# Optimization experiments

Hardware: AMD Instinct MI355X
Metric: run time of the kernel (lower is better)

## Reference

```python
import jax, jax.numpy as jnp
import numpy as np

BN_EPS = 1e-5


def three_nn(unknown, known):
    # squared pairwise distances via gemm form: ||u||^2 + ||k||^2 - 2 u.k
    # unknown: (B, n, 3), known: (B, m, 3) -> d: (B, n, m)
    u2 = jnp.sum(unknown * unknown, axis=-1, keepdims=True)          # (B, n, 1)
    k2 = jnp.sum(known * known, axis=-1)[:, None, :]                 # (B, 1, m)
    d = u2 + k2 - 2.0 * jnp.einsum('bnc,bmc->bnm', unknown, known)   # (B, n, m)
    neg_d, idx = jax.lax.top_k(-d, 3)                                # 3 smallest
    return -neg_d, idx                                               # (B,n,3), (B,n,3) int32


def three_interpolate(known_feats, idx, weight):
    # known_feats: (B, C, m), idx/weight: (B, n, 3) -> (B, C, n)
    g = jnp.take_along_axis(known_feats[:, :, None, :], idx[:, None, :, :], axis=3)  # (B,C,n,3)
    return jnp.sum(g * weight[:, None, :, :], axis=3)


def conv1x1(x, W, b):
    # x: (B, C_in, N), W: (C_out, C_in), b: (C_out,)
    return jnp.einsum('oc,bcn->bon', W, x) + b[None, :, None]


def batchnorm(x, gamma, beta):
    # training-mode BN over (B, N) per channel, biased variance
    mean = jnp.mean(x, axis=(0, 2), keepdims=True)
    var = jnp.mean((x - mean) ** 2, axis=(0, 2), keepdims=True)
    xn = (x - mean) * jax.lax.rsqrt(var + BN_EPS)
    return xn * gamma[None, :, None] + beta[None, :, None]


def setup_inputs() -> dict:
    key = jax.random.key(0)
    ks = jax.random.split(key, 16)
    B, n, m = 16, 4096, 1024
    C1, C2, C = 128, 256, 256  # in_channels, known feat channels (=mlp[0]), mlp width
    inp = {
        'unknown': jax.random.normal(ks[0], (B, n, 3), jnp.float32),
        'known': jax.random.normal(ks[1], (B, m, 3), jnp.float32),
        'unknow_feats': jax.random.normal(ks[2], (B, C1, n), jnp.float32),
        'known_feats': jax.random.normal(ks[3], (B, C2, m), jnp.float32),
        # mlp_unknow: Conv1d(C1->C) + BN (no relu)
        'Wu': jax.random.normal(ks[4], (C, C1), jnp.float32) * (1.0 / np.sqrt(C1)),
        'bu': jnp.zeros((C,), jnp.float32),
        'gu': jnp.ones((C,), jnp.float32),
        'betau': jnp.zeros((C,), jnp.float32),
        # mlp_convs[0]: Conv1d(C->C) + BN + relu
        'W1': jax.random.normal(ks[5], (C, C), jnp.float32) * (1.0 / np.sqrt(C)),
        'b1': jnp.zeros((C,), jnp.float32),
        'g1': jnp.ones((C,), jnp.float32),
        'beta1': jnp.zeros((C,), jnp.float32),
        # mlp_convs[1]: Conv1d(C->C) + BN + relu
        'W2': jax.random.normal(ks[6], (C, C), jnp.float32) * (1.0 / np.sqrt(C)),
        'b2': jnp.zeros((C,), jnp.float32),
        'g2': jnp.ones((C,), jnp.float32),
        'beta2': jnp.zeros((C,), jnp.float32),
    }
    return inp


def reference(unknown, known, unknow_feats, known_feats,
              Wu, bu, gu, betau, W1, b1, g1, beta1, W2, b2, g2, beta2):
    dist, idx = three_nn(unknown, known)            # squared dists (B,n,3)
    dist_recip = 1.0 / (dist + 1e-8)
    norm = jnp.sum(dist_recip, axis=2, keepdims=True)
    weight = dist_recip / norm
    interpolated = three_interpolate(known_feats, idx, weight)   # (B, 256, n)

    skip = batchnorm(conv1x1(unknow_feats, Wu, bu), gu, betau)   # (B, 256, n)
    x = interpolated + skip
    x = jax.nn.relu(batchnorm(conv1x1(x, W1, b1), g1, beta1))
    x = jax.nn.relu(batchnorm(conv1x1(x, W2, b2), g2, beta2))
    return x
```

## Files before the change

### kernel.cpp

```cpp
#include <hip/hip_runtime.h>
#include <hip/hip_bf16.h>
#include <cstddef>
#include <cstdint>

#define BATCH 16
#define NPTS  4096
#define MPTS  1024
#define PTOT  65536
#define C1    128
#define C2    256

typedef short bf16x8 __attribute__((ext_vector_type(8)));
typedef float f32x4  __attribute__((ext_vector_type(4)));
typedef unsigned int u32x4 __attribute__((ext_vector_type(4)));

static __device__ __forceinline__ float bf2f(unsigned int u16) {
    union { unsigned int i; float f; } v; v.i = u16 << 16; return v.f;
}
static __device__ __forceinline__ unsigned short f2bf(float f) {
    union { float f; unsigned int i; } v; v.f = f;
    unsigned int u = v.i;
    return (unsigned short)((u + 0x7FFFu + ((u >> 16) & 1u)) >> 16);
}

static __device__ __forceinline__ void st_wt_b128(void* p, u32x4 v) {
    asm volatile("global_store_dwordx4 %0, %1, off sc0 sc1" :: "v"(p), "v"(v) : "memory");
}
static __device__ __forceinline__ void st_wt_f128(void* p, f32x4 v) {
    asm volatile("global_store_dwordx4 %0, %1, off sc0 sc1" :: "v"(p), "v"(v) : "memory");
}
static __device__ __forceinline__ void st_wt_b32(void* p, unsigned v) {
    asm volatile("global_store_dword %0, %1, off sc0 sc1" :: "v"(p), "v"(v) : "memory");
}
static __device__ __forceinline__ void st_wt_b16(void* p, unsigned v) {
    asm volatile("global_store_short %0, %1, off sc0 sc1" :: "v"(p), "v"(v) : "memory");
}

template <int SWZ>
__global__ void k_transpose(const float* __restrict__ in, unsigned short* __restrict__ out,
                            int C, int N) {
    __shared__ float tile[64][65];
    int b  = blockIdx.z;
    int n0 = blockIdx.x * 64;
    int c0 = blockIdx.y * 64;
    const float* src = in + (size_t)b * C * N;
    unsigned short* dst = out + (size_t)b * N * C;
    int t  = threadIdx.x;
    int t4 = t >> 6;
    int tn = t & 63;
#pragma unroll
    for (int i = 0; i < 16; ++i) {
        int cc = i * 4 + t4;
        tile[cc][tn] = src[(size_t)(c0 + cc) * N + n0 + tn];
    }
    __syncthreads();
#pragma unroll
    for (int i = 0; i < 16; ++i) {
        int nn = i * 4 + t4;
        int p  = n0 + nn;
        int c  = c0 + tn;
        size_t off;
        if (SWZ) off = (size_t)p * C + (size_t)((((c >> 3) ^ (p & 7)) << 3) + (c & 7));
        else     off = (size_t)p * C + c;
        st_wt_b16(dst + off, (unsigned)f2bf(tile[tn][nn]));
    }
}

__global__ void k_cvt_pack(const float* __restrict__ in, unsigned short* __restrict__ out, int K) {
    int tid = blockIdx.x * 256 + threadIdx.x;
    if (tid >= 256 * K) return;
    int ch = tid / K, k = tid % K;
    int ks = k >> 5, lhi = (k >> 3) & 3, e = k & 7;
    int wv = ch >> 6, i = (ch >> 4) & 3, llo = ch & 15;
    int lane = lhi * 16 + llo;
    st_wt_b16(out + ((size_t)((ks * 16 + wv * 4 + i) * 64 + lane)) * 8 + e,
              (unsigned)f2bf(in[tid]));
}

static __device__ __forceinline__ bool nn_less(float da, int ia, float db, int ib) {
    return (da < db) || (da == db && ia < ib);
}

__global__ void k_three_nn(const float* __restrict__ unknown, const float* __restrict__ known,
                           int* __restrict__ idx_out, float* __restrict__ w_out) {
    __shared__ float4 kpt[MPTS + 8];
    int t  = threadIdx.x;
    int p0 = blockIdx.x * 32;
    int b  = p0 >> 12;
    const float* kb = known + (size_t)b * MPTS * 3;
    for (int i = t; i < MPTS; i += 256) {
        float x = kb[i * 3 + 0], y = kb[i * 3 + 1], z = kb[i * 3 + 2];
        float dd = __fadd_rn(__fadd_rn(__fmul_rn(x, x), __fmul_rn(y, y)), __fmul_rn(z, z));
        float4 v; v.x = x; v.y = y; v.z = z; v.w = dd;
        kpt[i + (i >> 7)] = v;
    }
    __syncthreads();

    int q = t & 7;
    int p = p0 + (t >> 3);
    const float* up = unknown + (size_t)p * 3;
    float ux = up[0], uy = up[1], uz = up[2];
    float u2 = __fadd_rn(__fadd_rn(__fmul_rn(ux, ux), __fmul_rn(uy, uy)), __fmul_rn(uz, uz));

    float d0 = INFINITY, d1 = INFINITY, d2 = INFINITY;
    int   i0 = 0, i1 = 0, i2 = 0;
    int base = q * 129;
#pragma unroll 4
    for (int it = 0; it < 128; ++it) {
        float4 kp = kpt[base + it];
        float dot = __fadd_rn(__fadd_rn(__fmul_rn(ux, kp.x), __fmul_rn(uy, kp.y)),
                              __fmul_rn(uz, kp.z));
        float d = __fsub_rn(__fadd_rn(u2, kp.w), __fmul_rn(2.0f, dot));
        int k = q * 128 + it;
        if (d < d0)      { d2 = d1; i2 = i1; d1 = d0; i1 = i0; d0 = d; i0 = k; }
        else if (d < d1) { d2 = d1; i2 = i1; d1 = d;  i1 = k; }
        else if (d < d2) { d2 = d;  i2 = k; }
    }

#pragma unroll
    for (int m = 1; m <= 4; m <<= 1) {
        float e0 = __shfl_xor(d0, m, 64), e1 = __shfl_xor(d1, m, 64), e2 = __shfl_xor(d2, m, 64);
        int   j0 = __shfl_xor(i0, m, 64), j1 = __shfl_xor(i1, m, 64), j2 = __shfl_xor(i2, m, 64);
        float a0 = d0, a1 = d1, a2 = d2; int x0 = i0, x1 = i1, x2 = i2;
        float b0 = e0, b1 = e1, b2 = e2; int y0 = j0, y1 = j1, y2 = j2;
        bool tk = nn_less(a0, x0, b0, y0);
        d0 = tk ? a0 : b0; i0 = tk ? x0 : y0;
        float na0 = tk ? a1 : a0; int nx0 = tk ? x1 : x0;
        float na1 = tk ? a2 : a1; int nx1 = tk ? x2 : x1;
        float nb0 = tk ? b0 : b1; int ny0 = tk ? y0 : y1;
        float nb1 = tk ? b1 : b2; int ny1 = tk ? y1 : y2;
        tk = nn_less(na0, nx0, nb0, ny0);
        d1 = tk ? na0 : nb0; i1 = tk ? nx0 : ny0;
        float ma0 = tk ? na1 : na0; int mx0 = tk ? nx1 : nx0;
        float mb0 = tk ? nb0 : nb1; int my0 = tk ? ny0 : ny1;
        tk = nn_less(ma0, mx0, mb0, my0);
        d2 = tk ? ma0 : mb0; i2 = tk ? mx0 : my0;
    }

    if (q == 0) {
        float r0 = 1.0f / (d0 + 1e-8f), r1 = 1.0f / (d1 + 1e-8f), r2 = 1.0f / (d2 + 1e-8f);
        float norm = r0 + r1 + r2;
        size_t pg = (size_t)p;
        st_wt_b32(idx_out + pg * 3 + 0, (unsigned)i0);
        st_wt_b32(idx_out + pg * 3 + 1, (unsigned)i1);
        st_wt_b32(idx_out + pg * 3 + 2, (unsigned)i2);
        union { float f; unsigned u; } w0v, w1v, w2v;
        w0v.f = r0 / norm; w1v.f = r1 / norm; w2v.f = r2 / norm;
        st_wt_b32(w_out + pg * 3 + 0, w0v.u);
        st_wt_b32(w_out + pg * 3 + 1, w1v.u);
        st_wt_b32(w_out + pg * 3 + 2, w2v.u);
    }
}

template <int K, int MODE>
__global__ __launch_bounds__(256, 4) void k_gemm(
        const unsigned short* __restrict__ Wp,
        const unsigned short* __restrict__ X,
        const float* __restrict__ Xf,
        const unsigned short* __restrict__ kfT,
        const int* __restrict__ idx,
        const float* __restrict__ wgt,
        const float* __restrict__ bias,
        const float* __restrict__ aff_a,
        const float* __restrict__ aff_c,
        unsigned short* __restrict__ Y,
        float* __restrict__ partial) {
    constexpr int NK = K / 32;
    constexpr int TB = 16 * K * 2;
    __shared__ char smem[8192];

    const int t    = threadIdx.x;
    const int p0   = blockIdx.x * 16;
    const int wv   = t >> 6;
    const int lane = t & 63;
    const int lhi  = lane >> 4, llo = lane & 15;

    if (MODE == 0) {
        const char* src = (const char*)(X + (size_t)p0 * K);
        constexpr int ITERS = TB / (256 * 16);
#pragma unroll
        for (int i = 0; i < ITERS; ++i) {
            int off = (i * 256 + t) * 16;
            __builtin_amdgcn_global_load_lds(
                (const __attribute__((address_space(1))) unsigned int*)(src + off),
                (__attribute__((address_space(3))) unsigned int*)(smem + off),
                16, 0, 0);
        }
    } else if (MODE == 1) {
        constexpr int CPR = K / 8;
#pragma unroll
        for (int i = 0; i < (16 * CPR) / 256; ++i) {
            int f   = i * 256 + t;
            int row = f / CPR, qp = f % CPR;
            int col = qp ^ (row & 7);
            uint4 v = *(const uint4*)(X + (size_t)(p0 + row) * K + qp * 8);
            unsigned int w[4] = {v.x, v.y, v.z, v.w};
            float4 a0 = *(const float4*)(aff_a + col * 8);
            float4 a1 = *(const float4*)(aff_a + col * 8 + 4);
            float4 cc0 = *(const float4*)(aff_c + col * 8);
            float4 cc1 = *(const float4*)(aff_c + col * 8 + 4);
            float aa[8] = {a0.x, a0.y, a0.z, a0.w, a1.x, a1.y, a1.z, a1.w};
            float cc[8] = {cc0.x, cc0.y, cc0.z, cc0.w, cc1.x, cc1.y, cc1.z, cc1.w};
#pragma unroll
            for (int q2 = 0; q2 < 4; ++q2) {
                float lo = fmaxf(bf2f(w[q2] & 0xffff) * aa[q2 * 2]     + cc[q2 * 2],     0.0f);
                float hi = fmaxf(bf2f(w[q2] >> 16)    * aa[q2 * 2 + 1] + cc[q2 * 2 + 1], 0.0f);
                w[q2] = (unsigned int)f2bf(lo) | ((unsigned int)f2bf(hi) << 16);
            }
            uint4 o; o.x = w[0]; o.y = w[1]; o.z = w[2]; o.w = w[3];
            *(uint4*)(smem + row * (K * 2) + qp * 16) = o;
        }
    } else if (MODE == 2) {
        int c    = t >> 1;
        int half = (t & 1) * 8;
        int b    = p0 >> 12;
        const float* src = Xf + ((size_t)b * C1 + c) * NPTS + (p0 & 4095) + half;
        float4 v0 = *(const float4*)(src);
        float4 v1 = *(const float4*)(src + 4);
        float fv[8] = {v0.x, v0.y, v0.z, v0.w, v1.x, v1.y, v1.z, v1.w};
#pragma unroll
        for (int e = 0; e < 8; ++e) {
            int p = half + e;
            *(unsigned short*)(smem + p * (K * 2) +
                               ((((c >> 3) ^ (p & 7)) << 4) + (c & 7) * 2)) = f2bf(fv[e]);
        }
    } else {
        int pj  = t >> 4;
        int sub = t & 15;
        int p   = p0 + pj;
        int b   = p >> 12;
        int i0 = idx[p * 3 + 0], i1 = idx[p * 3 + 1], i2 = idx[p * 3 + 2];
        float w0 = wgt[p * 3 + 0], w1 = wgt[p * 3 + 1], w2 = wgt[p * 3 + 2];
        const unsigned short* kb = kfT + (size_t)b * MPTS * C2;
#pragma unroll
        for (int cc2 = 0; cc2 < 2; ++cc2) {
            int cc = sub * 2 + cc2;
            int cbase = cc * 8;
            u32x4 v0 = *(const u32x4*)(kb + (size_t)i0 * C2 + cbase);
            u32x4 v1 = *(const u32x4*)(kb + (size_t)i1 * C2 + cbase);
            u32x4 v2 = *(const u32x4*)(kb + (size_t)i2 * C2 + cbase);
            int pos = cc ^ (p & 7);
            u32x4 vy = *(const u32x4*)(X + (size_t)p * C2 + pos * 8);
            float4 a0 = *(const float4*)(aff_a + cbase);
            float4 a1 = *(const float4*)(aff_a + cbase + 4);
            float4 c0f = *(const float4*)(aff_c + cbase);
            float4 c1f = *(const float4*)(aff_c + cbase + 4);
            float aa[8] = {a0.x, a0.y, a0.z, a0.w, a1.x, a1.y, a1.z, a1.w};
            float cf[8] = {c0f.x, c0f.y, c0f.z, c0f.w, c1f.x, c1f.y, c1f.z, c1f.w};
            unsigned r[4];
#pragma unroll
            for (int qq = 0; qq < 4; ++qq) {
                float lo = w0 * bf2f(v0[qq] & 0xffff) + w1 * bf2f(v1[qq] & 0xffff)
                         + w2 * bf2f(v2[qq] & 0xffff)
                         + bf2f(vy[qq] & 0xffff) * aa[qq * 2] + cf[qq * 2];
                float hi = w0 * bf2f(v0[qq] >> 16) + w1 * bf2f(v1[qq] >> 16)
                         + w2 * bf2f(v2[qq] >> 16)
                         + bf2f(vy[qq] >> 16) * aa[qq * 2 + 1] + cf[qq * 2 + 1];
                r[qq] = (unsigned)f2bf(lo) | ((unsigned)f2bf(hi) << 16);
            }
            u32x4 vo; vo.x = r[0]; vo.y = r[1]; vo.z = r[2]; vo.w = r[3];
            *(u32x4*)(smem + pj * 512 + pos * 16) = vo;
        }
    }

    const unsigned short* wbase = Wp + ((size_t)(wv * 256) + lane) * 8;
    bf16x8 wA[4], wB[4];
#pragma unroll
    for (int i = 0; i < 4; ++i)
        wA[i] = *(const bf16x8*)(wbase + i * 512);

    __syncthreads();

    f32x4 acc[4];
#pragma unroll
    for (int i = 0; i < 4; ++i) acc[i] = (f32x4){0.f, 0.f, 0.f, 0.f};

#pragma unroll
    for (int ks = 0; ks < NK; ks += 2) {
#pragma unroll
        for (int i = 0; i < 4; ++i)
            wB[i] = *(const bf16x8*)(wbase + (size_t)(ks + 1) * 8192 + i * 512);
        {
            int cp = (ks * 4 + lhi) ^ (llo & 7);
            bf16x8 bb = *(const bf16x8*)(smem + llo * (K * 2) + cp * 16);
#pragma unroll
            for (int i = 0; i < 4; ++i)
                acc[i] = __builtin_amdgcn_mfma_f32_16x16x32_bf16(wA[i], bb, acc[i], 0, 0, 0);
        }
        if (ks + 2 < NK) {
#pragma unroll
            for (int i = 0; i < 4; ++i)
                wA[i] = *(const bf16x8*)(wbase + (size_t)(ks + 2) * 8192 + i * 512);
        }
        {
            int cp = ((ks + 1) * 4 + lhi) ^ (llo & 7);
            bf16x8 bb = *(const bf16x8*)(smem + llo * (K * 2) + cp * 16);
#pragma unroll
            for (int i = 0; i < 4; ++i)
                acc[i] = __builtin_amdgcn_mfma_f32_16x16x32_bf16(wB[i], bb, acc[i], 0, 0, 0);
        }
    }

    __syncthreads();
#pragma unroll
    for (int i = 0; i < 4; ++i) {
        int cbase = wv * 64 + i * 16 + lhi * 4;
        float4 bv = *(const float4*)(bias + cbase);
        int c8 = cbase >> 3, hf = lhi & 1;
        int row = llo;
        float y0 = acc[i][0] + bv.x;
        float y1 = acc[i][1] + bv.y;
        float y2 = acc[i][2] + bv.z;
        float y3 = acc[i][3] + bv.w;
        float s0 = y0, q0 = y0 * y0;
        float s1 = y1, q1 = y1 * y1;
        float s2 = y2, q2 = y2 * y2;
        float s3 = y3, q3 = y3 * y3;
        unsigned int lo = (unsigned int)f2bf(y0) | ((unsigned int)f2bf(y1) << 16);
        unsigned int hi = (unsigned int)f2bf(y2) | ((unsigned int)f2bf(y3) << 16);
        uint2 o; o.x = lo; o.y = hi;
        *(uint2*)(smem + row * 512 + ((c8 ^ (row & 7)) << 4) + hf * 8) = o;
#pragma unroll
        for (int m = 1; m <= 8; m <<= 1) {
            s0 += __shfl_xor(s0, m, 64); q0 += __shfl_xor(q0, m, 64);
            s1 += __shfl_xor(s1, m, 64); q1 += __shfl_xor(q1, m, 64);
            s2 += __shfl_xor(s2, m, 64); q2 += __shfl_xor(q2, m, 64);
            s3 += __shfl_xor(s3, m, 64); q3 += __shfl_xor(q3, m, 64);
        }
        if (llo == 0) {
            f32x4 sv = {s0, s1, s2, s3};
            f32x4 qv = {q0, q1, q2, q3};
            st_wt_f128(partial + (size_t)blockIdx.x * 512 + cbase, sv);
            st_wt_f128(partial + (size_t)blockIdx.x * 512 + 256 + cbase, qv);
        }
    }
    __syncthreads();
    {
        const char* ysrc = smem + t * 16;
        char* ydst = (char*)(Y + (size_t)p0 * 256) + t * 16;
        u32x4 v0 = *(const u32x4*)(ysrc);
        u32x4 v1 = *(const u32x4*)(ysrc + 4096);
        st_wt_b128(ydst, v0);
        st_wt_b128(ydst + 4096, v1);
    }
}

__global__ void k_red1(const float* __restrict__ partial, float* __restrict__ partA) {
    int t = threadIdx.x, g = blockIdx.x;
    float s = 0.f, q = 0.f;
#pragma unroll 8
    for (int i = 0; i < 64; ++i) {
        const float* pp = partial + (size_t)(g * 64 + i) * 512;
        s += pp[t]; q += pp[256 + t];
    }
    union { float f; unsigned u; } sv, qv; sv.f = s; qv.f = q;
    st_wt_b32(partA + g * 512 + t, sv.u);
    st_wt_b32(partA + g * 512 + 256 + t, qv.u);
}

__global__ void k_finalize(const float* __restrict__ partA, const float* __restrict__ gamma,
                           const float* __restrict__ beta, float* __restrict__ aff_a,
                           float* __restrict__ aff_c) {
    int c = threadIdx.x;
    float s = 0.f, q = 0.f;
#pragma unroll 8
    for (int i = 0; i < 64; ++i) { s += partA[i * 512 + c]; q += partA[i * 512 + 256 + c]; }
    float mean = s * (1.0f / PTOT);
    float var  = fmaxf(q * (1.0f / PTOT) - mean * mean, 0.0f);
    float a    = gamma[c] / sqrtf(var + 1e-5f);
    union { float f; unsigned u; } av, cv;
    av.f = a; cv.f = beta[c] - mean * a;
    st_wt_b32(aff_a + c, av.u);
    st_wt_b32(aff_c + c, cv.u);
}

__global__ void k_final(const unsigned short* __restrict__ Y2, const float* __restrict__ aff_a,
                        const float* __restrict__ aff_c, float* __restrict__ out) {
    __shared__ float tile[64][65];
    int p0 = blockIdx.x * 64;
    int c0 = blockIdx.y * 64;
    int t  = threadIdx.x;
    int t4 = t >> 6, t64 = t & 63;
#pragma unroll
    for (int i = 0; i < 16; ++i) {
        int r = i * 4 + t4;
        int p = p0 + r;
        int c = c0 + t64;
        float v = bf2f(Y2[(size_t)p * 256 + (((c >> 3) ^ (p & 7)) << 3) + (c & 7)])
                  * aff_a[c] + aff_c[c];
        tile[t64][r] = fmaxf(v, 0.0f);
    }
    __syncthreads();
    int b   = p0 >> 12;
    int pin = p0 & 4095;
#pragma unroll
    for (int i = 0; i < 16; ++i) {
        int cc = i * 4 + t4;
        __builtin_nontemporal_store(tile[cc][t64],
            out + ((size_t)b * 256 + c0 + cc) * 4096 + pin + t64);
    }
}

extern "C" void kernel_launch(void* const* d_in, const int* in_sizes, int n_in,
                              void* d_out, int out_size, void* d_ws, size_t ws_size,
                              hipStream_t stream) {
    const float* unknown = (const float*)d_in[0];
    const float* known   = (const float*)d_in[1];
    const float* ufeat   = (const float*)d_in[2];
    const float* kfeat   = (const float*)d_in[3];
    const float* Wu      = (const float*)d_in[4];
    const float* bu      = (const float*)d_in[5];
    const float* gu      = (const float*)d_in[6];
    const float* betau   = (const float*)d_in[7];
    const float* W1      = (const float*)d_in[8];
    const float* b1      = (const float*)d_in[9];
    const float* g1      = (const float*)d_in[10];
    const float* beta1   = (const float*)d_in[11];
    const float* W2      = (const float*)d_in[12];
    const float* b2      = (const float*)d_in[13];
    const float* g2      = (const float*)d_in[14];
    const float* beta2   = (const float*)d_in[15];
    float* out = (float*)d_out;

    char* ws = (char*)d_ws;
    unsigned short* reg0 = (unsigned short*)ws;
    unsigned short* ybuf = (unsigned short*)(ws + ((size_t)32 << 20));
    unsigned short* kfT  = (unsigned short*)(ws + ((size_t)64 << 20));
    unsigned short* Wub  = (unsigned short*)(ws + ((size_t)72 << 20));
    unsigned short* W1b  = Wub + 256 * 128;
    unsigned short* W2b  = W1b + 256 * 256;
    int*   idxb = (int*)(W2b + 256 * 256);
    float* wgtb = (float*)(idxb + (size_t)PTOT * 3);
    float* affa0 = wgtb + (size_t)PTOT * 3;
    float* affc0 = affa0 + 256;
    float* affa1 = affc0 + 256;
    float* affc1 = affa1 + 256;
    float* affa2 = affc1 + 256;
    float* affc2 = affa2 + 256;
    float* partA = affc2 + 256;
    float* part0  = (float*)ws;
    float* partD  = (float*)d_out;
    if (ws_size < ((size_t)75 << 20)) return;

    k_transpose<0><<<dim3(MPTS / 64, C2 / 64, BATCH), 256, 0, stream>>>(kfeat, kfT, C2, MPTS);
    k_cvt_pack<<<128, 256, 0, stream>>>(Wu, Wub, 128);
    k_cvt_pack<<<256, 256, 0, stream>>>(W1, W1b, 256);
    k_cvt_pack<<<256, 256, 0, stream>>>(W2, W2b, 256);

    k_three_nn<<<PTOT / 32, 256, 0, stream>>>(unknown, known, idxb, wgtb);

    k_gemm<C1, 2><<<PTOT / 16, 256, 0, stream>>>(Wub, nullptr, ufeat, nullptr, nullptr, nullptr,
                                                 bu, nullptr, nullptr, ybuf, part0);
    k_red1<<<64, 256, 0, stream>>>(part0, partA);
    k_finalize<<<1, 256, 0, stream>>>(partA, gu, betau, affa0, affc0);

    k_gemm<C2, 3><<<PTOT / 16, 256, 0, stream>>>(W1b, ybuf, nullptr, kfT, idxb, wgtb,
                                                 b1, affa0, affc0, reg0, partD);
    k_red1<<<64, 256, 0, stream>>>(partD, partA);
    k_finalize<<<1, 256, 0, stream>>>(partA, g1, beta1, affa1, affc1);

    k_gemm<C2, 1><<<PTOT / 16, 256, 0, stream>>>(W2b, reg0, nullptr, nullptr, nullptr, nullptr,
                                                 b2, affa1, affc1, ybuf, partD);
    k_red1<<<64, 256, 0, stream>>>(partD, partA);
    k_finalize<<<1, 256, 0, stream>>>(partA, g2, beta2, affa2, affc2);

    k_final<<<dim3(PTOT / 64, 4), 256, 0, stream>>>(ybuf, affa2, affc2, out);

    (void)in_sizes; (void)n_in; (void)out_size;
}
```

Baseline: 211.0 us.

## Merge weight-pack launches, fuse BN stat reduction with finalize, widen three_nn tiles

The three weight conversion launches become one kernel that picks its source by block index. Each BN reduction and finalize pair becomes a single kernel, where the last block (found with an atomic counter zeroed by a memset) computes the affine parameters. Together these remove several small kernel launches. three_nn now gives 64 points to each block and splits the known points into 4 lanes of 256 each instead of 8 of 128, which halves the shuffle-merge steps and the per-block smem loads but lengthens each thread's serial loop. The unused MODE 0 gemm path is dropped.

```diff
diff --git a/kernel.cpp b/kernel.cpp
--- a/kernel.cpp
+++ b/kernel.cpp
@@ -66,9 +66,17 @@
     }
 }
 
-__global__ void k_cvt_pack(const float* __restrict__ in, unsigned short* __restrict__ out, int K) {
-    int tid = blockIdx.x * 256 + threadIdx.x;
-    if (tid >= 256 * K) return;
+__global__ void k_cvt_pack_all(const float* __restrict__ Wu, const float* __restrict__ W1,
+                               const float* __restrict__ W2,
+                               unsigned short* __restrict__ Wub,
+                               unsigned short* __restrict__ W1b,
+                               unsigned short* __restrict__ W2b) {
+    int blk = blockIdx.x;
+    const float* in; unsigned short* out; int K, lb;
+    if (blk < 128)      { in = Wu; out = Wub; K = 128; lb = blk; }
+    else if (blk < 384) { in = W1; out = W1b; K = 256; lb = blk - 128; }
+    else                { in = W2; out = W2b; K = 256; lb = blk - 384; }
+    int tid = lb * 256 + threadIdx.x;
     int ch = tid / K, k = tid % K;
     int ks = k >> 5, lhi = (k >> 3) & 3, e = k & 7;
     int wv = ch >> 6, i = (ch >> 4) & 3, llo = ch & 15;
@@ -83,42 +91,42 @@
 
 __global__ void k_three_nn(const float* __restrict__ unknown, const float* __restrict__ known,
                            int* __restrict__ idx_out, float* __restrict__ w_out) {
-    __shared__ float4 kpt[MPTS + 8];
+    __shared__ float4 kpt[MPTS + 4];
     int t  = threadIdx.x;
-    int p0 = blockIdx.x * 32;
+    int p0 = blockIdx.x * 64;
     int b  = p0 >> 12;
     const float* kb = known + (size_t)b * MPTS * 3;
     for (int i = t; i < MPTS; i += 256) {
         float x = kb[i * 3 + 0], y = kb[i * 3 + 1], z = kb[i * 3 + 2];
         float dd = __fadd_rn(__fadd_rn(__fmul_rn(x, x), __fmul_rn(y, y)), __fmul_rn(z, z));
         float4 v; v.x = x; v.y = y; v.z = z; v.w = dd;
-        kpt[i + (i >> 7)] = v;
-    }
-    __syncthreads();
-
-    int q = t & 7;
-    int p = p0 + (t >> 3);
+        kpt[i + (i >> 8)] = v;
+    }
+    __syncthreads();
+
+    int q = t & 3;
+    int p = p0 + (t >> 2);
     const float* up = unknown + (size_t)p * 3;
     float ux = up[0], uy = up[1], uz = up[2];
     float u2 = __fadd_rn(__fadd_rn(__fmul_rn(ux, ux), __fmul_rn(uy, uy)), __fmul_rn(uz, uz));
 
     float d0 = INFINITY, d1 = INFINITY, d2 = INFINITY;
     int   i0 = 0, i1 = 0, i2 = 0;
-    int base = q * 129;
+    int base = q * 257;
 #pragma unroll 4
-    for (int it = 0; it < 128; ++it) {
+    for (int it = 0; it < 256; ++it) {
         float4 kp = kpt[base + it];
         float dot = __fadd_rn(__fadd_rn(__fmul_rn(ux, kp.x), __fmul_rn(uy, kp.y)),
                               __fmul_rn(uz, kp.z));
         float d = __fsub_rn(__fadd_rn(u2, kp.w), __fmul_rn(2.0f, dot));
-        int k = q * 128 + it;
+        int k = q * 256 + it;
         if (d < d0)      { d2 = d1; i2 = i1; d1 = d0; i1 = i0; d0 = d; i0 = k; }
         else if (d < d1) { d2 = d1; i2 = i1; d1 = d;  i1 = k; }
         else if (d < d2) { d2 = d;  i2 = k; }
     }
 
 #pragma unroll
-    for (int m = 1; m <= 4; m <<= 1) {
+    for (int m = 1; m <= 2; m <<= 1) {
         float e0 = __shfl_xor(d0, m, 64), e1 = __shfl_xor(d1, m, 64), e2 = __shfl_xor(d2, m, 64);
         int   j0 = __shfl_xor(i0, m, 64), j1 = __shfl_xor(i1, m, 64), j2 = __shfl_xor(i2, m, 64);
         float a0 = d0, a1 = d1, a2 = d2; int x0 = i0, x1 = i1, x2 = i2;
@@ -166,7 +174,6 @@
         unsigned short* __restrict__ Y,
         float* __restrict__ partial) {
     constexpr int NK = K / 32;
-    constexpr int TB = 16 * K * 2;
     __shared__ char smem[8192];
 
     const int t    = threadIdx.x;
@@ -175,18 +182,7 @@
     const int lane = t & 63;
     const int lhi  = lane >> 4, llo = lane & 15;
 
-    if (MODE == 0) {
-        const char* src = (const char*)(X + (size_t)p0 * K);
-        constexpr int ITERS = TB / (256 * 16);
-#pragma unroll
-        for (int i = 0; i < ITERS; ++i) {
-            int off = (i * 256 + t) * 16;
-            __builtin_amdgcn_global_load_lds(
-                (const __attribute__((address_space(1))) unsigned int*)(src + off),
-                (__attribute__((address_space(3))) unsigned int*)(smem + off),
-                16, 0, 0);
-        }
-    } else if (MODE == 1) {
+    if (MODE == 1) {
         constexpr int CPR = K / 8;
 #pragma unroll
         for (int i = 0; i < (16 * CPR) / 256; ++i) {
@@ -345,7 +341,10 @@
     }
 }
 
-__global__ void k_red1(const float* __restrict__ partial, float* __restrict__ partA) {
+__global__ void k_stats(const float* __restrict__ partial, float* __restrict__ partA,
+                        const float* __restrict__ gamma, const float* __restrict__ beta,
+                        float* __restrict__ aff_a, float* __restrict__ aff_c,
+                        unsigned* __restrict__ counter) {
     int t = threadIdx.x, g = blockIdx.x;
     float s = 0.f, q = 0.f;
 #pragma unroll 8
@@ -353,25 +352,27 @@
         const float* pp = partial + (size_t)(g * 64 + i) * 512;
         s += pp[t]; q += pp[256 + t];
     }
-    union { float f; unsigned u; } sv, qv; sv.f = s; qv.f = q;
-    st_wt_b32(partA + g * 512 + t, sv.u);
-    st_wt_b32(partA + g * 512 + 256 + t, qv.u);
-}
-
-__global__ void k_finalize(const float* __restrict__ partA, const float* __restrict__ gamma,
-                           const float* __restrict__ beta, float* __restrict__ aff_a,
-                           float* __restrict__ aff_c) {
-    int c = threadIdx.x;
-    float s = 0.f, q = 0.f;
+    partA[g * 512 + t]       = s;
+    partA[g * 512 + 256 + t] = q;
+    __threadfence();
+    __syncthreads();
+    __shared__ unsigned lastv;
+    if (t == 0) lastv = atomicAdd(counter, 1u);
+    __syncthreads();
+    if (lastv == 63u) {
+        __threadfence();
+        float s2 = 0.f, q2 = 0.f;
 #pragma unroll 8
-    for (int i = 0; i < 64; ++i) { s += partA[i * 512 + c]; q += partA[i * 512 + 256 + c]; }
-    float mean = s * (1.0f / PTOT);
-    float var  = fmaxf(q * (1.0f / PTOT) - mean * mean, 0.0f);
-    float a    = gamma[c] / sqrtf(var + 1e-5f);
-    union { float f; unsigned u; } av, cv;
-    av.f = a; cv.f = beta[c] - mean * a;
-    st_wt_b32(aff_a + c, av.u);
-    st_wt_b32(aff_c + c, cv.u);
+        for (int i = 0; i < 64; ++i) {
+            s2 += partA[i * 512 + t];
+            q2 += partA[i * 512 + 256 + t];
+        }
+        float mean = s2 * (1.0f / PTOT);
+        float var  = fmaxf(q2 * (1.0f / PTOT) - mean * mean, 0.0f);
+        float a    = gamma[t] / sqrtf(var + 1e-5f);
+        aff_a[t] = a;
+        aff_c[t] = beta[t] - mean * a;
+    }
 }
 
 __global__ void k_final(const unsigned short* __restrict__ Y2, const float* __restrict__ aff_a,
@@ -438,31 +439,29 @@
     float* affa2 = affc1 + 256;
     float* affc2 = affa2 + 256;
     float* partA = affc2 + 256;
+    unsigned* cnts = (unsigned*)(partA + 64 * 512);
     float* part0  = (float*)ws;
     float* partD  = (float*)d_out;
     if (ws_size < ((size_t)75 << 20)) return;
 
+    hipMemsetAsync(cnts, 0, 12, stream);
+
     k_transpose<0><<<dim3(MPTS / 64, C2 / 64, BATCH), 256, 0, stream>>>(kfeat, kfT, C2, MPTS);
-    k_cvt_pack<<<128, 256, 0, stream>>>(Wu, Wub, 128);
-    k_cvt_pack<<<256, 256, 0, stream>>>(W1, W1b, 256);
-    k_cvt_pack<<<256, 256, 0, stream>>>(W2, W2b, 256);
-
-    k_three_nn<<<PTOT / 32, 256, 0, stream>>>(unknown, known, idxb, wgtb);
+    k_cvt_pack_all<<<640, 256, 0, stream>>>(Wu, W1, W2, Wub, W1b, W2b);
+
+    k_three_nn<<<PTOT / 64, 256, 0, stream>>>(unknown, known, idxb, wgtb);
 
     k_gemm<C1, 2><<<PTOT / 16, 256, 0, stream>>>(Wub, nullptr, ufeat, nullptr, nullptr, nullptr,
                                                  bu, nullptr, nullptr, ybuf, part0);
-    k_red1<<<64, 256, 0, stream>>>(part0, partA);
-    k_finalize<<<1, 256, 0, stream>>>(partA, gu, betau, affa0, affc0);
+    k_stats<<<64, 256, 0, stream>>>(part0, partA, gu, betau, affa0, affc0, cnts + 0);
 
     k_gemm<C2, 3><<<PTOT / 16, 256, 0, stream>>>(W1b, ybuf, nullptr, kfT, idxb, wgtb,
                                                  b1, affa0, affc0, reg0, partD);
-    k_red1<<<64, 256, 0, stream>>>(partD, partA);
-    k_finalize<<<1, 256, 0, stream>>>(partA, g1, beta1, affa1, affc1);
+    k_stats<<<64, 256, 0, stream>>>(partD, partA, g1, beta1, affa1, affc1, cnts + 1);
 
     k_gemm<C2, 1><<<PTOT / 16, 256, 0, stream>>>(W2b, reg0, nullptr, nullptr, nullptr, nullptr,
                                                  b2, affa1, affc1, ybuf, partD);
-    k_red1<<<64, 256, 0, stream>>>(partD, partA);
-    k_finalize<<<1, 256, 0, stream>>>(partA, g2, beta2, affa2, affc2);
+    k_stats<<<64, 256, 0, stream>>>(partD, partA, g2, beta2, affa2, affc2, cnts + 2);
 
     k_final<<<dim3(PTOT / 64, 4), 256, 0, stream>>>(ybuf, affa2, affc2, out);
 
```

Result: slower. 228.7 us (+8.4%).
